# Kernel tuning notes

Measured on AMD Instinct MI355X. Metric: run time of the kernel, lower is better.

Reference implementation:

```python
import jax, jax.numpy as jnp
import numpy as np

N_HEAD = 16
G_HEADS = 2
D_HEAD = 64
D_MODEL = 1024
HEAD_RATIO = N_HEAD // G_HEADS  # 8
QK_DIM = G_HEADS * D_HEAD       # 128
SCALE = 1.0 / D_HEAD ** 0.5
LN_EPS = 1e-5


def _rel_shift(x):
    # x: [qlen, rlen, B, n] -- Transformer-XL relative shift
    q, r = x.shape[0], x.shape[1]
    x_pad = jnp.pad(x, ((0, 0), (1, 0), (0, 0), (0, 0)))      # [q, r+1, B, n]
    x_pad = x_pad.reshape(r + 1, q, *x.shape[2:])[1:]          # drop first row
    return x_pad.reshape(q, r, *x.shape[2:])


def setup_inputs() -> dict:
    key = jax.random.key(0)
    ks = jax.random.split(key, 9)
    qlen, bsz, levels = 1024, 4, 3
    w = jax.random.normal(ks[0], (qlen, bsz, D_MODEL), jnp.float32)
    r = jax.random.normal(ks[1], (qlen, D_MODEL), jnp.float32)
    r_w_bias = jax.random.normal(ks[2], (G_HEADS, D_HEAD), jnp.float32) * 0.02
    r_r_bias = jax.random.normal(ks[3], (G_HEADS, D_HEAD), jnp.float32) * 0.02
    masks = jax.random.uniform(ks[4], (qlen, qlen, levels), jnp.float32)
    W_qkv = jax.random.normal(ks[5], (2 * QK_DIM + N_HEAD * D_HEAD, D_MODEL), jnp.float32) * 0.02
    W_r = jax.random.normal(ks[6], (QK_DIM, D_MODEL), jnp.float32) * 0.02
    mask_proj = jnp.ones((levels, N_HEAD), jnp.float32)
    W_o = jax.random.normal(ks[7], (D_MODEL, N_HEAD * D_HEAD), jnp.float32) * 0.02
    ln_gamma = jnp.ones((D_MODEL,), jnp.float32)
    ln_beta = jnp.zeros((D_MODEL,), jnp.float32)
    return dict(w=w, r=r, r_w_bias=r_w_bias, r_r_bias=r_r_bias, masks=masks,
                W_qkv=W_qkv, W_r=W_r, mask_proj=mask_proj, W_o=W_o,
                ln_gamma=ln_gamma, ln_beta=ln_beta)


def reference(w, r, r_w_bias, r_r_bias, masks, W_qkv, W_r, mask_proj, W_o, ln_gamma, ln_beta):
    qlen, bsz, _ = w.shape
    rlen = r.shape[0]
    N = qlen  # no mems: klen == qlen == rlen

    w_heads = w @ W_qkv.T                                   # [q, B, 1280]
    r_head_k = (r @ W_r.T).reshape(rlen, G_HEADS, D_HEAD)   # [r, gH, d]
    w_head_q = w_heads[..., :QK_DIM].reshape(qlen, bsz, G_HEADS, D_HEAD)
    w_head_k = w_heads[..., QK_DIM:2 * QK_DIM].reshape(qlen, bsz, G_HEADS, D_HEAD)
    w_head_v = w_heads[..., 2 * QK_DIM:].reshape(qlen, bsz, N_HEAD, D_HEAD)

    AC = jnp.einsum('ibnd,jbnd->ijbn', w_head_q + r_w_bias, w_head_k)
    BD = jnp.einsum('ibnd,jnd->ijbn', w_head_q + r_r_bias, r_head_k)
    BD = _rel_shift(BD)
    attn_score = (AC + BD) * SCALE                           # [N, N, B, gH]

    # per-head mask mixing ('full' projection)
    attn = jnp.transpose(attn_score, (2, 3, 0, 1))           # [B, gH, N, N]
    mw = (masks @ mask_proj).reshape(N, N, G_HEADS, HEAD_RATIO)
    mw = jnp.transpose(mw, (2, 0, 1, 3))                     # [gH, N, N, hr]
    attn = attn[..., None] * mw[None]                        # [B, gH, N, N, hr]
    attn = jnp.transpose(attn, (0, 1, 4, 2, 3)).reshape(bsz, N_HEAD, N, N)
    attn_score = jnp.transpose(attn, (2, 3, 0, 1))           # [N, N, B, H]

    attn_prob = jax.nn.softmax(attn_score, axis=1)
    attn_vec = jnp.einsum('ijbn,jbnd->ibnd', attn_prob, w_head_v)
    attn_vec = attn_vec.reshape(qlen, bsz, N_HEAD * D_HEAD)
    attn_out = attn_vec @ W_o.T                              # [q, B, d_model]

    # post-LN residual
    x = w + attn_out
    mu = jnp.mean(x, axis=-1, keepdims=True)
    var = jnp.mean((x - mu) ** 2, axis=-1, keepdims=True)
    return (x - mu) * jax.lax.rsqrt(var + LN_EPS) * ln_gamma + ln_beta
```

## Files before the change

kernel.cpp:

```cpp
#include <hip/hip_runtime.h>
#include <cstddef>
#include <cstdint>

#define QLEN   1024
#define SCALE  0.125f
#define LN_EPS 1e-5f
#define DMODEL 1024

typedef __bf16 bf16x8 __attribute__((ext_vector_type(8)));
typedef __bf16 bf16x4 __attribute__((ext_vector_type(4)));
typedef float  f32x4  __attribute__((ext_vector_type(4)));

__device__ __forceinline__ void load16_lds(const void* g, void* l) {
  __builtin_amdgcn_global_load_lds(
      (const __attribute__((address_space(1))) unsigned int*)g,
      (__attribute__((address_space(3))) unsigned int*)l, 16, 0, 0);
}

__device__ __forceinline__ void bar_lds() {
  asm volatile("s_waitcnt lgkmcnt(0)" ::: "memory");
  __builtin_amdgcn_s_barrier();
  asm volatile("" ::: "memory");
}

__global__ __launch_bounds__(256) void cast_all(
    const float* __restrict__ w, __bf16* __restrict__ w_bf,
    const float* __restrict__ Wqkv, __bf16* __restrict__ Wqkv_bf,
    const float* __restrict__ r, __bf16* __restrict__ r_bf,
    const float* __restrict__ Wr, __bf16* __restrict__ Wr_bf,
    const float* __restrict__ Wo, __bf16* __restrict__ Wo_bf)
{
  int blk = blockIdx.x;
  const float* in; __bf16* out;
  if (blk < 2048)      { in = w;    out = w_bf;    }
  else if (blk < 2688) { blk -= 2048; in = Wqkv; out = Wqkv_bf; }
  else if (blk < 3200) { blk -= 2688; in = r;    out = r_bf;    }
  else if (blk < 3264) { blk -= 3200; in = Wr;   out = Wr_bf;   }
  else                 { blk -= 3264; in = Wo;   out = Wo_bf;   }
  const size_t i = ((size_t)blk * 256 + threadIdx.x) * 8;
  const float4 a = *(const float4*)&in[i];
  const float4 b = *(const float4*)&in[i + 4];
  bf16x8 o;
  o[0] = (__bf16)a.x; o[1] = (__bf16)a.y; o[2] = (__bf16)a.z; o[3] = (__bf16)a.w;
  o[4] = (__bf16)b.x; o[5] = (__bf16)b.y; o[6] = (__bf16)b.z; o[7] = (__bf16)b.w;
  *(bf16x8*)&out[i] = o;
}

__global__ __launch_bounds__(256) void gemm_proj(
    const __bf16* __restrict__ w_bf, const __bf16* __restrict__ Wqkv_bf,
    const __bf16* __restrict__ r_bf, const __bf16* __restrict__ Wr_bf,
    const float* __restrict__ rwb, const float* __restrict__ rrb,
    __bf16* __restrict__ Qw, __bf16* __restrict__ Qr,
    __bf16* __restrict__ Kb, __bf16* __restrict__ Vt,
    __bf16* __restrict__ Rb)
{
  __shared__ __bf16 Asl[128 * 32];
  __shared__ __bf16 Bsl[64 * 32];
  const int blk = blockIdx.x;
  const bool isR = blk >= 640;
  const __bf16 *A, *B;
  int m0, n0;
  if (!isR) { A = w_bf; B = Wqkv_bf; n0 = (blk % 20) * 64; m0 = (blk / 20) * 128; }
  else      { const int k = blk - 640; A = r_bf; B = Wr_bf;
              n0 = (k % 2) * 64; m0 = (k / 2) * 128; }

  const int tid = threadIdx.x, lane = tid & 63, wv = tid >> 6;
  const int lr = lane & 15, kq = lane >> 4;
  const int srow  = wv * 16 + (lane >> 2);
  const int sslot = lane & 3;
  const int sg0 = (sslot - ((srow >> 1) & 3)) & 3;
  const int sg1 = (sslot - (((srow + 64) >> 1) & 3)) & 3;
  const __bf16* Ag = A + (size_t)(m0 + srow) * 1024;
  const __bf16* Bg = B + (size_t)(n0 + srow) * 1024;
  __bf16* Al = &Asl[srow * 32 + sslot * 8];
  __bf16* Bl = &Bsl[srow * 32 + sslot * 8];

  f32x4 acc[2][4];
#pragma unroll
  for (int mt = 0; mt < 2; ++mt)
#pragma unroll
    for (int nt = 0; nt < 4; ++nt)
      acc[mt][nt] = (f32x4){0.f, 0.f, 0.f, 0.f};

  for (int k0 = 0; k0 < 1024; k0 += 32) {
    load16_lds(Ag + k0 + sg0 * 8, Al);
    load16_lds(Ag + (size_t)64 * 1024 + k0 + sg1 * 8, Al + 64 * 32);
    load16_lds(Bg + k0 + sg0 * 8, Bl);
    __syncthreads();
    bf16x8 af[2], bfr[4];
#pragma unroll
    for (int mt = 0; mt < 2; ++mt) {
      const int row = wv * 32 + mt * 16 + lr;
      af[mt] = *(const bf16x8*)&Asl[row * 32 + ((kq + (row >> 1)) & 3) * 8];
    }
#pragma unroll
    for (int nt = 0; nt < 4; ++nt) {
      const int row = nt * 16 + lr;
      bfr[nt] = *(const bf16x8*)&Bsl[row * 32 + ((kq + (row >> 1)) & 3) * 8];
    }
#pragma unroll
    for (int mt = 0; mt < 2; ++mt)
#pragma unroll
      for (int nt = 0; nt < 4; ++nt)
        acc[mt][nt] = __builtin_amdgcn_mfma_f32_16x16x32_bf16(
            af[mt], bfr[nt], acc[mt][nt], 0, 0, 0);
    __syncthreads();
  }

#pragma unroll
  for (int mt = 0; mt < 2; ++mt) {
    const int row0 = m0 + wv * 32 + mt * 16 + kq * 4;
#pragma unroll
    for (int nt = 0; nt < 4; ++nt) {
      const int gcol = n0 + nt * 16 + lr;
      const f32x4 c = acc[mt][nt];
      if (isR) {
        const int g = gcol >> 6, d = gcol & 63;
#pragma unroll
        for (int reg = 0; reg < 4; ++reg)
          Rb[(size_t)g * 65536 + (size_t)(row0 + reg) * 64 + d] = (__bf16)c[reg];
      } else if (gcol < 128) {
        const int g = gcol >> 6, d = gcol & 63;
        const float bw = rwb[gcol], br = rrb[gcol];
#pragma unroll
        for (int reg = 0; reg < 4; ++reg) {
          const int row = row0 + reg, i = row >> 2, b = row & 3;
          const size_t o = (size_t)(b * 2 + g) * 65536 + (size_t)i * 64 + d;
          Qw[o] = (__bf16)(c[reg] + bw);
          Qr[o] = (__bf16)(c[reg] + br);
        }
      } else if (gcol < 256) {
        const int lc = gcol - 128, g = lc >> 6, d = lc & 63;
#pragma unroll
        for (int reg = 0; reg < 4; ++reg) {
          const int row = row0 + reg, i = row >> 2, b = row & 3;
          Kb[(size_t)(b * 2 + g) * 65536 + (size_t)i * 64 + d] = (__bf16)c[reg];
        }
      } else {
        const int lc = gcol - 256, h = lc >> 6, d = lc & 63;
#pragma unroll
        for (int reg = 0; reg < 4; ++reg) {
          const int row = row0 + reg, i = row >> 2, b = row & 3;
          Vt[((size_t)((b * 16 + h) * 64 + d)) * 1024 + i] = (__bf16)c[reg];
        }
      }
    }
  }
}

__global__ __launch_bounds__(256) void gemm_wo(
    const __bf16* __restrict__ A, const __bf16* __restrict__ B,
    float* __restrict__ C)
{
  __shared__ __bf16 Asl[128 * 32];
  __shared__ __bf16 Bsl[64 * 32];
  const int m0 = blockIdx.y * 128, n0 = blockIdx.x * 64;
  const int tid = threadIdx.x, lane = tid & 63, wv = tid >> 6;
  const int lr = lane & 15, kq = lane >> 4;
  const int srow  = wv * 16 + (lane >> 2);
  const int sslot = lane & 3;
  const int sg0 = (sslot - ((srow >> 1) & 3)) & 3;
  const int sg1 = (sslot - (((srow + 64) >> 1) & 3)) & 3;
  const __bf16* Ag = A + (size_t)(m0 + srow) * 1024;
  const __bf16* Bg = B + (size_t)(n0 + srow) * 1024;
  __bf16* Al = &Asl[srow * 32 + sslot * 8];
  __bf16* Bl = &Bsl[srow * 32 + sslot * 8];

  f32x4 acc[2][4];
#pragma unroll
  for (int mt = 0; mt < 2; ++mt)
#pragma unroll
    for (int nt = 0; nt < 4; ++nt)
      acc[mt][nt] = (f32x4){0.f, 0.f, 0.f, 0.f};

  for (int k0 = 0; k0 < 1024; k0 += 32) {
    load16_lds(Ag + k0 + sg0 * 8, Al);
    load16_lds(Ag + (size_t)64 * 1024 + k0 + sg1 * 8, Al + 64 * 32);
    load16_lds(Bg + k0 + sg0 * 8, Bl);
    __syncthreads();
    bf16x8 af[2], bfr[4];
#pragma unroll
    for (int mt = 0; mt < 2; ++mt) {
      const int row = wv * 32 + mt * 16 + lr;
      af[mt] = *(const bf16x8*)&Asl[row * 32 + ((kq + (row >> 1)) & 3) * 8];
    }
#pragma unroll
    for (int nt = 0; nt < 4; ++nt) {
      const int row = nt * 16 + lr;
      bfr[nt] = *(const bf16x8*)&Bsl[row * 32 + ((kq + (row >> 1)) & 3) * 8];
    }
#pragma unroll
    for (int mt = 0; mt < 2; ++mt)
#pragma unroll
      for (int nt = 0; nt < 4; ++nt)
        acc[mt][nt] = __builtin_amdgcn_mfma_f32_16x16x32_bf16(
            af[mt], bfr[nt], acc[mt][nt], 0, 0, 0);
    __syncthreads();
  }

#pragma unroll
  for (int mt = 0; mt < 2; ++mt) {
    const int row0 = m0 + wv * 32 + mt * 16 + kq * 4;
#pragma unroll
    for (int nt = 0; nt < 4; ++nt) {
      const int col = n0 + nt * 16 + lr;
      const f32x4 c = acc[mt][nt];
#pragma unroll
      for (int reg = 0; reg < 4; ++reg)
        C[(size_t)(row0 + reg) * 1024 + col] = c[reg];
    }
  }
}

__global__ __launch_bounds__(256) void gemm64_bf16(
    const __bf16* __restrict__ Qw, const __bf16* __restrict__ Qr,
    const __bf16* __restrict__ Kb, const __bf16* __restrict__ Rb,
    __bf16* __restrict__ AC, __bf16* __restrict__ BDo)
{
  __shared__ __bf16 Asl[128 * 64];
  __shared__ __bf16 Bsl[128 * 64];
  const int tid = threadIdx.x, lane = tid & 63, wv = tid >> 6;
  const int which = blockIdx.z & 1, bat = blockIdx.z >> 1;
  const int m0 = blockIdx.y * 128, n0 = blockIdx.x * 128;
  const __bf16* Ap = (which ? Qr : Qw) + (size_t)bat * 65536;
  const __bf16* Bp = which ? (Rb + (size_t)(bat & 1) * 65536)
                           : (Kb + (size_t)bat * 65536);
  __bf16* Cp = (which ? BDo : AC) + (size_t)bat * 1048576;

#pragma unroll
  for (int p = 0; p < 4; ++p) {
    const int row = wv * 32 + p * 8 + (lane >> 3);
    const int s = lane & 7;
    const int gc = (s - (row & 7)) & 7;
    load16_lds(Ap + (size_t)(m0 + row) * 64 + gc * 8, &Asl[row * 64 + s * 8]);
    load16_lds(Bp + (size_t)(n0 + row) * 64 + gc * 8, &Bsl[row * 64 + s * 8]);
  }
  __syncthreads();

  const int lr = lane & 15, kq = lane >> 4;
  const int wm = (wv >> 1) * 64, wn = (wv & 1) * 64;
  f32x4 acc[4][4];
#pragma unroll
  for (int mt = 0; mt < 4; ++mt)
#pragma unroll
    for (int nt = 0; nt < 4; ++nt)
      acc[mt][nt] = (f32x4){0.f, 0.f, 0.f, 0.f};

#pragma unroll
  for (int ks = 0; ks < 2; ++ks) {
    const int c = ks * 4 + kq;
    bf16x8 af[4], bfr[4];
#pragma unroll
    for (int mt = 0; mt < 4; ++mt) {
      const int row = wm + mt * 16 + lr;
      af[mt] = *(const bf16x8*)&Asl[row * 64 + ((c + (row & 7)) & 7) * 8];
    }
#pragma unroll
    for (int nt = 0; nt < 4; ++nt) {
      const int row = wn + nt * 16 + lr;
      bfr[nt] = *(const bf16x8*)&Bsl[row * 64 + ((c + (row & 7)) & 7) * 8];
    }
#pragma unroll
    for (int mt = 0; mt < 4; ++mt)
#pragma unroll
      for (int nt = 0; nt < 4; ++nt)
        acc[mt][nt] = __builtin_amdgcn_mfma_f32_16x16x32_bf16(
            af[mt], bfr[nt], acc[mt][nt], 0, 0, 0);
  }

#pragma unroll
  for (int mt = 0; mt < 4; ++mt) {
    const int row0 = m0 + wm + mt * 16 + kq * 4;
#pragma unroll
    for (int nt = 0; nt < 4; ++nt) {
      const int col = n0 + wn + nt * 16 + lr;
      const f32x4 cc = acc[mt][nt];
#pragma unroll
      for (int reg = 0; reg < 4; ++reg)
        Cp[(size_t)(row0 + reg) * 1024 + col] = (__bf16)cc[reg];
    }
  }
}

__global__ __launch_bounds__(256) void prep2(
    const __bf16* __restrict__ AC, const __bf16* __restrict__ BDm,
    __bf16* __restrict__ Tg,
    const float* __restrict__ masks, const float* __restrict__ mproj,
    __bf16* __restrict__ Mh)
{
  const int tid = threadIdx.x;
  if (blockIdx.x < 2048) {
    const int blk = blockIdx.x;
    const size_t bg = blk >> 8;
    const int i = (blk & 255) * 4 + (tid >> 6);
    const int lane = tid & 63;
    const __bf16* ACr = AC + bg * 1048576 + (size_t)i * 1024;
    const __bf16* BDb = BDm + bg * 1048576;
    __bf16* Tr = Tg + bg * 1048576 + (size_t)i * 1024;
#pragma unroll
    for (int c2 = 0; c2 < 4; ++c2) {
      const int j0 = c2 * 256 + lane * 4;
      const bf16x4 ac4 = *(const bf16x4*)&ACr[j0];
      bf16x4 o;
#pragma unroll
      for (int k = 0; k < 4; ++k) {
        const int j = j0 + k;
        float bd;
        if (j <= i)          bd = (float)BDb[(size_t)i * 1024 + (j + QLEN - 1 - i)];
        else if (j == i + 1) bd = 0.f;
        else                 bd = (float)BDb[(size_t)(i + 1) * 1024 + (j - i - 2)];
        o[k] = (__bf16)(((float)ac4[k] + bd) * SCALE);
      }
      *(bf16x4*)&Tr[j0] = o;
    }
  } else {
    const int blk = blockIdx.x - 2048;
    const size_t ij0 = ((size_t)blk * 256 + tid) * 4;
    const float4 a = *(const float4*)&masks[ij0 * 3];
    const float4 b = *(const float4*)&masks[ij0 * 3 + 4];
    const float4 c = *(const float4*)&masks[ij0 * 3 + 8];
    const float m0[4] = {a.x, a.w, b.z, c.y};
    const float m1[4] = {a.y, b.x, b.w, c.z};
    const float m2[4] = {a.z, b.y, c.x, c.w};
#pragma unroll
    for (int h = 0; h < 16; ++h) {
      const float p0 = mproj[h], p1 = mproj[16 + h], p2 = mproj[32 + h];
      bf16x4 o;
#pragma unroll
      for (int k = 0; k < 4; ++k)
        o[k] = (__bf16)(m0[k] * p0 + m1[k] * p1 + m2[k] * p2);
      *(bf16x4*)&Mh[(size_t)h * 1048576 + ij0] = o;
    }
  }
}

__global__ __launch_bounds__(256, 8) void attn7(
    const __bf16* __restrict__ Tg, const __bf16* __restrict__ Mh,
    const __bf16* __restrict__ Vt, __bf16* __restrict__ av)
{
  __shared__ __bf16 P[2][16 * 256];
  __shared__ float rinvS[16];
  const int tid = threadIdx.x;
  const int i0 = blockIdx.x * 16;
  const int h = blockIdx.y, b = blockIdx.z;
  const int g = h >> 3;
  const size_t bg = (size_t)(b * 2 + g);
  const int r = tid >> 4, li = tid & 15;
  const __bf16* Trow = Tg + bg * 1048576 + (size_t)(i0 + r) * 1024;
  const __bf16* Mrow = Mh + (size_t)h * 1048576 + (size_t)(i0 + r) * 1024;

  const int lane = tid & 63, wv = tid >> 6;
  const int m = lane & 15, kq = lane >> 4;
  const __bf16* vbase = Vt + ((size_t)((b * 16 + h) * 64 + wv * 16 + m)) * 1024 + kq * 8;

  float sum = 0.f;
  f32x4 acc[4];
#pragma unroll
  for (int u = 0; u < 4; ++u) acc[u] = (f32x4){0.f, 0.f, 0.f, 0.f};

  for (int ch = 0; ch < 4; ++ch) {
    const int cb = ch & 1;
#pragma unroll
    for (int q = 0; q < 2; ++q) {
      const int jc = q * 128 + li * 8;
      const bf16x8 t8 = *(const bf16x8*)&Trow[ch * 256 + jc];
      const bf16x8 m8 = *(const bf16x8*)&Mrow[ch * 256 + jc];
      const int slot = (jc >> 3) ^ (r & 7);
      bf16x8 p8;
#pragma unroll
      for (int k = 0; k < 8; ++k) {
        const float e = __expf((float)t8[k] * (float)m8[k]);
        sum += e;
        p8[k] = (__bf16)e;
      }
      *(bf16x8*)&P[cb][r * 256 + slot * 8] = p8;
    }
    bar_lds();
#pragma unroll
    for (int ks = 0; ks < 8; ++ks) {
      const int c = ks * 4 + kq;
      const bf16x8 a = *(const bf16x8*)&P[cb][m * 256 + ((c ^ (m & 7)) << 3)];
      const bf16x8 vv = *(const bf16x8*)&vbase[(ch * 8 + ks) * 32];
      acc[ks & 3] = __builtin_amdgcn_mfma_f32_16x16x32_bf16(a, vv, acc[ks & 3], 0, 0, 0);
    }
  }

  sum += __shfl_xor(sum, 1);
  sum += __shfl_xor(sum, 2);
  sum += __shfl_xor(sum, 4);
  sum += __shfl_xor(sum, 8);
  if (li == 0) rinvS[r] = 1.f / sum;
  __syncthreads();

  const f32x4 accf = (acc[0] + acc[1]) + (acc[2] + acc[3]);
#pragma unroll
  for (int reg = 0; reg < 4; ++reg) {
    const int row = kq * 4 + reg;
    av[((size_t)(i0 + row) * 4 + b) * 1024 + h * 64 + wv * 16 + m] =
        (__bf16)(accf[reg] * rinvS[row]);
  }
}

__global__ __launch_bounds__(256) void ln_kernel(
    const float* __restrict__ w, const float* __restrict__ ao,
    const float* __restrict__ gamma, const float* __restrict__ beta,
    float* __restrict__ out)
{
  const int tid = threadIdx.x;
  const size_t base = (size_t)blockIdx.x * DMODEL;
  __shared__ float red[256];
  float x[4];
  float s = 0.f;
#pragma unroll
  for (int p = 0; p < 4; ++p) {
    const int c = tid + p * 256;
    x[p] = w[base + c] + ao[base + c];
    s += x[p];
  }
  red[tid] = s; __syncthreads();
  for (int off = 128; off > 0; off >>= 1) {
    if (tid < off) red[tid] += red[tid + off];
    __syncthreads();
  }
  const float mu = red[0] * (1.f / DMODEL);
  __syncthreads();
  float s2 = 0.f;
#pragma unroll
  for (int p = 0; p < 4; ++p) { const float t = x[p] - mu; s2 += t * t; }
  red[tid] = s2; __syncthreads();
  for (int off = 128; off > 0; off >>= 1) {
    if (tid < off) red[tid] += red[tid + off];
    __syncthreads();
  }
  const float rs = rsqrtf(red[0] * (1.f / DMODEL) + LN_EPS);
#pragma unroll
  for (int p = 0; p < 4; ++p) {
    const int c = tid + p * 256;
    out[base + c] = (x[p] - mu) * rs * gamma[c] + beta[c];
  }
}

extern "C" void kernel_launch(void* const* d_in, const int* in_sizes, int n_in,
                              void* d_out, int out_size, void* d_ws, size_t ws_size,
                              hipStream_t stream)
{
  const float* w     = (const float*)d_in[0];
  const float* r     = (const float*)d_in[1];
  const float* rwb   = (const float*)d_in[2];
  const float* rrb   = (const float*)d_in[3];
  const float* masks = (const float*)d_in[4];
  const float* Wqkv  = (const float*)d_in[5];
  const float* Wr    = (const float*)d_in[6];
  const float* mproj = (const float*)d_in[7];
  const float* Wo    = (const float*)d_in[8];
  const float* gam   = (const float*)d_in[9];
  const float* bet   = (const float*)d_in[10];
  float* out = (float*)d_out;

  float* ws = (float*)d_ws;
  __bf16* w_bf    = (__bf16*)(ws);
  __bf16* Wqkv_bf = (__bf16*)(ws + 2097152);
  __bf16* r_bf    = (__bf16*)(ws + 2752512);
  __bf16* Wr_bf   = (__bf16*)(ws + 3276800);
  __bf16* Qw      = (__bf16*)(ws + 3342336);
  __bf16* Qr      = (__bf16*)(ws + 3604480);
  __bf16* Kb      = (__bf16*)(ws + 3866624);
  __bf16* Rb      = (__bf16*)(ws + 4128768);
  __bf16* Mh      = (__bf16*)(ws);
  __bf16* AC_bf   = (__bf16*)(ws + 8388608);
  float*  ao      = ws + 8388608;
  __bf16* BD_bf   = (__bf16*)(ws + 12582912);
  __bf16* Tg      = (__bf16*)(ws + 16777216);
  __bf16* Vt      = (__bf16*)(ws + 20971520);
  __bf16* av_bf   = (__bf16*)(ws + 23068672);
  __bf16* Wo_bf   = (__bf16*)(ws + 25165824);

  cast_all<<<3776, 256, 0, stream>>>(w, w_bf, Wqkv, Wqkv_bf, r, r_bf,
                                     Wr, Wr_bf, Wo, Wo_bf);
  gemm_proj<<<656, 256, 0, stream>>>(
      w_bf, Wqkv_bf, r_bf, Wr_bf, rwb, rrb, Qw, Qr, Kb, Vt, Rb);
  gemm64_bf16<<<dim3(8, 8, 16), 256, 0, stream>>>(Qw, Qr, Kb, Rb, AC_bf, BD_bf);
  prep2<<<3072, 256, 0, stream>>>(AC_bf, BD_bf, Tg, masks, mproj, Mh);
  attn7<<<dim3(64, 16, 4), 256, 0, stream>>>(Tg, Mh, Vt, av_bf);
  gemm_wo<<<dim3(16, 32), 256, 0, stream>>>(av_bf, Wo_bf, ao);
  ln_kernel<<<4096, 256, 0, stream>>>(w, ao, gam, bet, out);
}
```

Measured before the change: 260.8 us.

## Double attention row tile to 32 and prefetch T/M and V into registers

The attention-probability x V kernel now handles 32 query rows per block instead of 16, so each V fragment loaded from global memory feeds two MFMA row tiles. This halves the V traffic per output. It also software-prefetches the next chunk's T and mask values into registers while the current chunk's exps and MFMAs run, and loads V for a chunk ahead of the barrier. The cost is more registers and twice the LDS, with launch bounds lowered to 4 blocks per CU, which reduces occupancy.

```diff
diff --git a/kernel.cpp b/kernel.cpp
--- a/kernel.cpp
+++ b/kernel.cpp
@@ -334,70 +334,95 @@
   }
 }
 
-__global__ __launch_bounds__(256, 8) void attn7(
+__global__ __launch_bounds__(256, 4) void attn8(
     const __bf16* __restrict__ Tg, const __bf16* __restrict__ Mh,
     const __bf16* __restrict__ Vt, __bf16* __restrict__ av)
 {
-  __shared__ __bf16 P[2][16 * 256];
-  __shared__ float rinvS[16];
+  __shared__ __bf16 P[2][32 * 256];
+  __shared__ float rinvS[32];
   const int tid = threadIdx.x;
-  const int i0 = blockIdx.x * 16;
+  const int i0 = blockIdx.x * 32;
   const int h = blockIdx.y, b = blockIdx.z;
   const int g = h >> 3;
   const size_t bg = (size_t)(b * 2 + g);
-  const int r = tid >> 4, li = tid & 15;
-  const __bf16* Trow = Tg + bg * 1048576 + (size_t)(i0 + r) * 1024;
-  const __bf16* Mrow = Mh + (size_t)h * 1048576 + (size_t)(i0 + r) * 1024;
+  const int r = tid >> 3, li = tid & 7;
+  const __bf16* Trow = Tg + bg * 1048576 + (size_t)(i0 + r) * 1024 + li * 8;
+  const __bf16* Mrow = Mh + (size_t)h * 1048576 + (size_t)(i0 + r) * 1024 + li * 8;
 
   const int lane = tid & 63, wv = tid >> 6;
   const int m = lane & 15, kq = lane >> 4;
   const __bf16* vbase = Vt + ((size_t)((b * 16 + h) * 64 + wv * 16 + m)) * 1024 + kq * 8;
 
   float sum = 0.f;
-  f32x4 acc[4];
-#pragma unroll
-  for (int u = 0; u < 4; ++u) acc[u] = (f32x4){0.f, 0.f, 0.f, 0.f};
+  f32x4 acc[2][2];
+#pragma unroll
+  for (int mt = 0; mt < 2; ++mt)
+#pragma unroll
+    for (int u = 0; u < 2; ++u)
+      acc[mt][u] = (f32x4){0.f, 0.f, 0.f, 0.f};
+
+  bf16x8 t[4], mk[4], v[8];
+#pragma unroll
+  for (int q = 0; q < 4; ++q) {
+    t[q]  = *(const bf16x8*)&Trow[q * 64];
+    mk[q] = *(const bf16x8*)&Mrow[q * 64];
+  }
 
   for (int ch = 0; ch < 4; ++ch) {
     const int cb = ch & 1;
 #pragma unroll
-    for (int q = 0; q < 2; ++q) {
-      const int jc = q * 128 + li * 8;
-      const bf16x8 t8 = *(const bf16x8*)&Trow[ch * 256 + jc];
-      const bf16x8 m8 = *(const bf16x8*)&Mrow[ch * 256 + jc];
-      const int slot = (jc >> 3) ^ (r & 7);
+    for (int ks = 0; ks < 8; ++ks)
+      v[ks] = *(const bf16x8*)&vbase[(ch * 8 + ks) * 32];
+#pragma unroll
+    for (int q = 0; q < 4; ++q) {
       bf16x8 p8;
+      float s0 = 0.f;
 #pragma unroll
       for (int k = 0; k < 8; ++k) {
-        const float e = __expf((float)t8[k] * (float)m8[k]);
-        sum += e;
+        const float e = __expf((float)t[q][k] * (float)mk[q][k]);
+        s0 += e;
         p8[k] = (__bf16)e;
       }
+      sum += s0;
+      const int slot = (q * 8 + li) ^ (r & 7);
       *(bf16x8*)&P[cb][r * 256 + slot * 8] = p8;
+    }
+    if (ch < 3) {
+#pragma unroll
+      for (int q = 0; q < 4; ++q) {
+        t[q]  = *(const bf16x8*)&Trow[(ch + 1) * 256 + q * 64];
+        mk[q] = *(const bf16x8*)&Mrow[(ch + 1) * 256 + q * 64];
+      }
     }
     bar_lds();
 #pragma unroll
     for (int ks = 0; ks < 8; ++ks) {
       const int c = ks * 4 + kq;
-      const bf16x8 a = *(const bf16x8*)&P[cb][m * 256 + ((c ^ (m & 7)) << 3)];
-      const bf16x8 vv = *(const bf16x8*)&vbase[(ch * 8 + ks) * 32];
-      acc[ks & 3] = __builtin_amdgcn_mfma_f32_16x16x32_bf16(a, vv, acc[ks & 3], 0, 0, 0);
+#pragma unroll
+      for (int mt = 0; mt < 2; ++mt) {
+        const int R = mt * 16 + m;
+        const bf16x8 a = *(const bf16x8*)&P[cb][R * 256 + ((c ^ (R & 7)) << 3)];
+        acc[mt][ks & 1] = __builtin_amdgcn_mfma_f32_16x16x32_bf16(
+            a, v[ks], acc[mt][ks & 1], 0, 0, 0);
+      }
     }
   }
 
   sum += __shfl_xor(sum, 1);
   sum += __shfl_xor(sum, 2);
   sum += __shfl_xor(sum, 4);
-  sum += __shfl_xor(sum, 8);
   if (li == 0) rinvS[r] = 1.f / sum;
   __syncthreads();
 
-  const f32x4 accf = (acc[0] + acc[1]) + (acc[2] + acc[3]);
-#pragma unroll
-  for (int reg = 0; reg < 4; ++reg) {
-    const int row = kq * 4 + reg;
-    av[((size_t)(i0 + row) * 4 + b) * 1024 + h * 64 + wv * 16 + m] =
-        (__bf16)(accf[reg] * rinvS[row]);
+#pragma unroll
+  for (int mt = 0; mt < 2; ++mt) {
+    const f32x4 accf = acc[mt][0] + acc[mt][1];
+#pragma unroll
+    for (int reg = 0; reg < 4; ++reg) {
+      const int row = mt * 16 + kq * 4 + reg;
+      av[((size_t)(i0 + row) * 4 + b) * 1024 + h * 64 + wv * 16 + m] =
+          (__bf16)(accf[reg] * rinvS[row]);
+    }
   }
 }
 
@@ -481,7 +506,7 @@
       w_bf, Wqkv_bf, r_bf, Wr_bf, rwb, rrb, Qw, Qr, Kb, Vt, Rb);
   gemm64_bf16<<<dim3(8, 8, 16), 256, 0, stream>>>(Qw, Qr, Kb, Rb, AC_bf, BD_bf);
   prep2<<<3072, 256, 0, stream>>>(AC_bf, BD_bf, Tg, masks, mproj, Mh);
-  attn7<<<dim3(64, 16, 4), 256, 0, stream>>>(Tg, Mh, Vt, av_bf);
+  attn8<<<dim3(32, 16, 4), 256, 0, stream>>>(Tg, Mh, Vt, av_bf);
   gemm_wo<<<dim3(16, 32), 256, 0, stream>>>(av_bf, Wo_bf, ao);
   ln_kernel<<<4096, 256, 0, stream>>>(w, ao, gam, bet, out);
 }
```

After: 237.1 us. 9.1% less time.
